# Kernel optimization log

Hardware: AMD Instinct MI355X
Metric: run time of the kernel (lower is better)

Reference implementation:

```python
import jax, jax.numpy as jnp
import numpy as np

B, N, IMG_DIM, EMBED = 32, 1024, 2048, 1024


def setup_inputs() -> dict:
    key = jax.random.key(0)
    k1, k2, k3, k4, k5 = jax.random.split(key, 5)
    r1 = np.sqrt(6.0) / np.sqrt(IMG_DIM + EMBED)  # xavier range for ws1 (code uses r, same formula)
    return {
        "images": jax.random.normal(k1, (B, N, IMG_DIM), dtype=jnp.float32),
        "cap_embs": jax.random.normal(k2, (B, EMBED), dtype=jnp.float32),
        # valid lengths per sample in [N//2, N] to keep rows non-empty (ragged)
        "lengths_img": jax.random.randint(k3, (B,), N // 2, N + 1, dtype=jnp.int32),
        "ws1_w": jax.random.uniform(k4, (EMBED, IMG_DIM), minval=-r1, maxval=r1, dtype=jnp.float32),
        "ws1_b": jnp.zeros((EMBED,), dtype=jnp.float32),
        "fc_w": jax.random.uniform(k5, (EMBED, EMBED), minval=-r1, maxval=r1, dtype=jnp.float32),
        "fc_b": jnp.zeros((EMBED,), dtype=jnp.float32),
    }


def reference(images, cap_embs, lengths_img, ws1_w, ws1_b, fc_w, fc_b):
    # image_feature = ws1(images): [B, N, E]
    feat = jnp.einsum("bnd,ed->bne", images, ws1_w) + ws1_b
    # cross_attention: bmm([B,N,E], [B,E,1]) -> scores [B, N]
    scores = jnp.einsum("bne,be->bn", feat, cap_embs)
    # per-sample variable-length softmax over the first lengths_img[i] frames,
    # zeros elsewhere (torch loop writes into a zeros buffer)
    mask = jnp.arange(N)[None, :] < lengths_img[:, None]        # [B, N]
    logits = jnp.where(mask, scores, jnp.float32(-1e30))
    w = jax.nn.softmax(logits, axis=1)
    w = jnp.where(mask, w, 0.0)
    # torch uses .data + new Variable -> attention weights are detached
    w = jax.lax.stop_gradient(w)
    # out = bmm(feat^T [B,E,N], w [B,N,1]).squeeze() -> [B, E]
    out = jnp.einsum("bne,bn->be", feat, w)
    features = out @ fc_w.T + fc_b                               # fc: [B, E]
    # l2norm over dim=1
    features = features / jnp.sqrt(jnp.sum(features * features, axis=1))[:, None]
    return features, w[:, :, None]  # attn_weights [B, N, 1]
```

## Files before the change

kernel.cpp:

```cpp
#include <hip/hip_runtime.h>
#include <hip/hip_bf16.h>
#include <math.h>

#define BB 32
#define NN 1024
#define DD 2048
#define EE 1024

__global__ __launch_bounds__(256) void k1_partial(const float* __restrict__ W,
                                                  const float* __restrict__ cap,
                                                  float* __restrict__ part) {
    int ec = blockIdx.x >> 3;
    int dslab = blockIdx.x & 7;
    int d = dslab * 256 + threadIdx.x;
    float acc[BB];
#pragma unroll
    for (int b = 0; b < BB; ++b) acc[b] = 0.f;
    int e0 = ec * 64;
    for (int ee = 0; ee < 64; ++ee) {
        int e = e0 + ee;
        float wv = W[e * DD + d];
#pragma unroll
        for (int b = 0; b < BB; ++b) acc[b] += cap[b * EE + e] * wv;
    }
#pragma unroll
    for (int b = 0; b < BB; ++b) part[(ec * BB + b) * DD + d] = acc[b];
}

__global__ __launch_bounds__(256) void k1_reduce(const float* __restrict__ part,
                                                 float* __restrict__ v) {
    int idx = blockIdx.x * 256 + threadIdx.x;
    float s = 0.f;
#pragma unroll
    for (int ec = 0; ec < 16; ++ec) s += part[ec * 65536 + idx];
    v[idx] = s;
}

__global__ __launch_bounds__(256) void k2_scores(const float4* __restrict__ img4,
                                                 const float4* __restrict__ v4,
                                                 float* __restrict__ scores) {
    int wid = threadIdx.x >> 6;
    int lane = threadIdx.x & 63;
    int r = blockIdx.x * 4 + wid;
    int b = r >> 10;
    const float4* ip = img4 + (size_t)r * 512;
    const float4* vp = v4 + b * 512;
    float acc = 0.f;
#pragma unroll
    for (int it = 0; it < 8; ++it) {
        float4 a = ip[it * 64 + lane];
        float4 c = vp[it * 64 + lane];
        acc += a.x * c.x + a.y * c.y + a.z * c.z + a.w * c.w;
    }
#pragma unroll
    for (int off = 32; off > 0; off >>= 1) acc += __shfl_xor(acc, off, 64);
    if (lane == 0) scores[r] = acc;
}

__global__ __launch_bounds__(256) void k3_softmax(const float* __restrict__ scores,
                                                  const int* __restrict__ lengths,
                                                  float* __restrict__ wout,
                                                  int* __restrict__ sig_idx,
                                                  float* __restrict__ sig_w,
                                                  int* __restrict__ sig_cnt) {
    __shared__ float red[256];
    __shared__ int scnt;
    int b = blockIdx.x, tid = threadIdx.x;
    int len = lengths[b];
    float s[4];
    bool valid[4];
    float mx = -3.0e38f;
#pragma unroll
    for (int k = 0; k < 4; ++k) {
        int n = tid + k * 256;
        valid[k] = n < len;
        s[k] = valid[k] ? scores[b * NN + n] : -3.0e38f;
        mx = fmaxf(mx, s[k]);
    }
    if (tid == 0) scnt = 0;
    red[tid] = mx;
    __syncthreads();
    for (int o = 128; o > 0; o >>= 1) {
        if (tid < o) red[tid] = fmaxf(red[tid], red[tid + o]);
        __syncthreads();
    }
    mx = red[0];
    __syncthreads();
    float e[4], sum = 0.f;
#pragma unroll
    for (int k = 0; k < 4; ++k) {
        e[k] = valid[k] ? expf(s[k] - mx) : 0.f;
        sum += e[k];
    }
    red[tid] = sum;
    __syncthreads();
    for (int o = 128; o > 0; o >>= 1) {
        if (tid < o) red[tid] += red[tid + o];
        __syncthreads();
    }
    float inv = 1.0f / red[0];
#pragma unroll
    for (int k = 0; k < 4; ++k) {
        int n = tid + k * 256;
        float wv = e[k] * inv;
        wout[b * NN + n] = wv;
        if (wv > 1e-12f) {
            int p = atomicAdd(&scnt, 1);
            sig_idx[b * NN + p] = n;
            sig_w[b * NN + p] = wv;
        }
    }
    __syncthreads();
    if (tid == 0) sig_cnt[b] = scnt;
}

__global__ __launch_bounds__(256) void k4_u(const float* __restrict__ images,
                                            const int* __restrict__ sig_idx,
                                            const float* __restrict__ sig_w,
                                            const int* __restrict__ sig_cnt,
                                            float* __restrict__ u) {
    int b = blockIdx.x >> 3;
    int dslab = blockIdx.x & 7;
    int d = dslab * 256 + threadIdx.x;
    int cnt = sig_cnt[b];
    const float* ib = images + (size_t)b * NN * DD;
    float acc = 0.f;
    for (int i = 0; i < cnt; ++i) {
        float wv = sig_w[b * NN + i];
        int n = sig_idx[b * NN + i];
        acc += wv * ib[(size_t)n * DD + d];
    }
    u[b * DD + d] = acc;
}

__global__ __launch_bounds__(256) void k5_fc(const float4* __restrict__ W4,
                                             const float4* __restrict__ x4,
                                             const float* __restrict__ bias,
                                             float* __restrict__ out, int nit) {
    int wid = threadIdx.x >> 6;
    int lane = threadIdx.x & 63;
    int e = blockIdx.x * 4 + wid;
    int rowq = nit * 64;
    const float4* wp = W4 + (size_t)e * rowq;
    float acc[BB];
#pragma unroll
    for (int b = 0; b < BB; ++b) acc[b] = 0.f;
    for (int it = 0; it < nit; ++it) {
        float4 wv = wp[it * 64 + lane];
#pragma unroll
        for (int b = 0; b < BB; ++b) {
            float4 uv = x4[b * rowq + it * 64 + lane];
            acc[b] += wv.x * uv.x + wv.y * uv.y + wv.z * uv.z + wv.w * uv.w;
        }
    }
    float bv = bias[e];
#pragma unroll
    for (int b = 0; b < BB; ++b) {
        float r = acc[b];
#pragma unroll
        for (int off = 32; off > 0; off >>= 1) r += __shfl_xor(r, off, 64);
        if (lane == 0) out[b * EE + e] = r + bv;
    }
}

__global__ __launch_bounds__(256) void k7_norm(const float* __restrict__ fpre,
                                               float* __restrict__ outF) {
    __shared__ float red[256];
    int b = blockIdx.x, tid = threadIdx.x;
    float f[4];
    float ss = 0.f;
#pragma unroll
    for (int k = 0; k < 4; ++k) {
        f[k] = fpre[b * EE + tid + k * 256];
        ss += f[k] * f[k];
    }
    red[tid] = ss;
    __syncthreads();
    for (int o = 128; o > 0; o >>= 1) {
        if (tid < o) red[tid] += red[tid + o];
        __syncthreads();
    }
    float inv = 1.0f / sqrtf(red[0]);
#pragma unroll
    for (int k = 0; k < 4; ++k) outF[b * EE + tid + k * 256] = f[k] * inv;
}

extern "C" void kernel_launch(void* const* d_in, const int* in_sizes, int n_in,
                              void* d_out, int out_size, void* d_ws, size_t ws_size,
                              hipStream_t stream) {
    const float* images = (const float*)d_in[0];
    const float* cap    = (const float*)d_in[1];
    const int*   lens   = (const int*)d_in[2];
    const float* ws1_w  = (const float*)d_in[3];
    const float* ws1_b  = (const float*)d_in[4];
    const float* fc_w   = (const float*)d_in[5];
    const float* fc_b   = (const float*)d_in[6];
    float* out = (float*)d_out;

    float* wsf    = (float*)d_ws;
    float* part   = wsf;
    float* v      = part + 1048576;
    float* scores = v + 65536;
    float* u      = scores + 32768;
    float* fc1    = u + 65536;
    float* fpre   = fc1 + 32768;
    float* sig_w  = fpre + 32768;
    int*   sig_idx = (int*)(sig_w + 32768);
    int*   sig_cnt = sig_idx + 32768;
    float* w_out  = out + BB * EE;

    k1_partial<<<128, 256, 0, stream>>>(ws1_w, cap, part);
    k1_reduce<<<256, 256, 0, stream>>>(part, v);
    k2_scores<<<8192, 256, 0, stream>>>((const float4*)images, (const float4*)v, scores);
    k3_softmax<<<32, 256, 0, stream>>>(scores, lens, w_out, sig_idx, sig_w, sig_cnt);
    k4_u<<<256, 256, 0, stream>>>(images, sig_idx, sig_w, sig_cnt, u);
    k5_fc<<<256, 256, 0, stream>>>((const float4*)ws1_w, (const float4*)u, ws1_b, fc1, 8);
    k5_fc<<<256, 256, 0, stream>>>((const float4*)fc_w, (const float4*)fc1, fc_b, fpre, 4);
    k7_norm<<<32, 256, 0, stream>>>(fpre, out);
}
```

Measured before the change: 452.2 us.

## Fuse softmax with weighted row gather and batch four rows per wave in scores

The softmax kernel and the weighted image-row accumulation are merged into one kernel per batch sample. The significant-row indices and weights now stay in shared memory instead of going through global memory, and one kernel launch is removed. Separately, each wave in the score kernel now computes four rows and keeps the query vector in registers, which cuts redundant loads of v and raises per-wave work. The risk is that the fused kernel runs only 32 blocks, each walking all 8 column slabs in turn, so the gather parallelism drops if many rows are significant.

```diff
diff --git a/kernel.cpp b/kernel.cpp
--- a/kernel.cpp
+++ b/kernel.cpp
@@ -41,29 +41,36 @@
                                                  float* __restrict__ scores) {
     int wid = threadIdx.x >> 6;
     int lane = threadIdx.x & 63;
-    int r = blockIdx.x * 4 + wid;
-    int b = r >> 10;
-    const float4* ip = img4 + (size_t)r * 512;
+    int w = blockIdx.x * 4 + wid;
+    int r0 = w * 4;
+    int b = r0 >> 10;
     const float4* vp = v4 + b * 512;
-    float acc = 0.f;
-#pragma unroll
-    for (int it = 0; it < 8; ++it) {
-        float4 a = ip[it * 64 + lane];
-        float4 c = vp[it * 64 + lane];
-        acc += a.x * c.x + a.y * c.y + a.z * c.z + a.w * c.w;
-    }
-#pragma unroll
-    for (int off = 32; off > 0; off >>= 1) acc += __shfl_xor(acc, off, 64);
-    if (lane == 0) scores[r] = acc;
-}
-
-__global__ __launch_bounds__(256) void k3_softmax(const float* __restrict__ scores,
-                                                  const int* __restrict__ lengths,
-                                                  float* __restrict__ wout,
-                                                  int* __restrict__ sig_idx,
-                                                  float* __restrict__ sig_w,
-                                                  int* __restrict__ sig_cnt) {
+    float4 vr[8];
+#pragma unroll
+    for (int it = 0; it < 8; ++it) vr[it] = vp[it * 64 + lane];
+#pragma unroll
+    for (int j = 0; j < 4; ++j) {
+        const float4* ip = img4 + (size_t)(r0 + j) * 512;
+        float acc = 0.f;
+#pragma unroll
+        for (int it = 0; it < 8; ++it) {
+            float4 a = ip[it * 64 + lane];
+            acc += a.x * vr[it].x + a.y * vr[it].y + a.z * vr[it].z + a.w * vr[it].w;
+        }
+#pragma unroll
+        for (int off = 32; off > 0; off >>= 1) acc += __shfl_xor(acc, off, 64);
+        if (lane == 0) scores[r0 + j] = acc;
+    }
+}
+
+__global__ __launch_bounds__(256) void k34(const float* __restrict__ scores,
+                                           const int* __restrict__ lengths,
+                                           const float* __restrict__ images,
+                                           float* __restrict__ wout,
+                                           float* __restrict__ u) {
     __shared__ float red[256];
+    __shared__ float sw[NN];
+    __shared__ int sn[NN];
     __shared__ int scnt;
     int b = blockIdx.x, tid = threadIdx.x;
     int len = lengths[b];
@@ -106,31 +113,21 @@
         wout[b * NN + n] = wv;
         if (wv > 1e-12f) {
             int p = atomicAdd(&scnt, 1);
-            sig_idx[b * NN + p] = n;
-            sig_w[b * NN + p] = wv;
+            sn[p] = n;
+            sw[p] = wv;
         }
     }
     __syncthreads();
-    if (tid == 0) sig_cnt[b] = scnt;
-}
-
-__global__ __launch_bounds__(256) void k4_u(const float* __restrict__ images,
-                                            const int* __restrict__ sig_idx,
-                                            const float* __restrict__ sig_w,
-                                            const int* __restrict__ sig_cnt,
-                                            float* __restrict__ u) {
-    int b = blockIdx.x >> 3;
-    int dslab = blockIdx.x & 7;
-    int d = dslab * 256 + threadIdx.x;
-    int cnt = sig_cnt[b];
+    int cnt = scnt;
     const float* ib = images + (size_t)b * NN * DD;
-    float acc = 0.f;
-    for (int i = 0; i < cnt; ++i) {
-        float wv = sig_w[b * NN + i];
-        int n = sig_idx[b * NN + i];
-        acc += wv * ib[(size_t)n * DD + d];
-    }
-    u[b * DD + d] = acc;
+#pragma unroll
+    for (int c = 0; c < 8; ++c) {
+        int d = c * 256 + tid;
+        float acc = 0.f;
+        for (int i = 0; i < cnt; ++i)
+            acc += sw[i] * ib[(size_t)sn[i] * DD + d];
+        u[b * DD + d] = acc;
+    }
 }
 
 __global__ __launch_bounds__(256) void k5_fc(const float4* __restrict__ W4,
@@ -204,16 +201,12 @@
     float* u      = scores + 32768;
     float* fc1    = u + 65536;
     float* fpre   = fc1 + 32768;
-    float* sig_w  = fpre + 32768;
-    int*   sig_idx = (int*)(sig_w + 32768);
-    int*   sig_cnt = sig_idx + 32768;
     float* w_out  = out + BB * EE;
 
     k1_partial<<<128, 256, 0, stream>>>(ws1_w, cap, part);
     k1_reduce<<<256, 256, 0, stream>>>(part, v);
-    k2_scores<<<8192, 256, 0, stream>>>((const float4*)images, (const float4*)v, scores);
-    k3_softmax<<<32, 256, 0, stream>>>(scores, lens, w_out, sig_idx, sig_w, sig_cnt);
-    k4_u<<<256, 256, 0, stream>>>(images, sig_idx, sig_w, sig_cnt, u);
+    k2_scores<<<2048, 256, 0, stream>>>((const float4*)images, (const float4*)v, scores);
+    k34<<<32, 256, 0, stream>>>(scores, lens, images, w_out, u);
     k5_fc<<<256, 256, 0, stream>>>((const float4*)ws1_w, (const float4*)u, ws1_b, fc1, 8);
     k5_fc<<<256, 256, 0, stream>>>((const float4*)fc_w, (const float4*)fc1, fc_b, fpre, 4);
     k7_norm<<<32, 256, 0, stream>>>(fpre, out);
```

Measured after the change: 467.1 us. +3.3%, slower.
